# Optimization experiments

Hardware: AMD Instinct MI355X
Metric: run time of the kernel (lower is better)

Reference implementation:

```python
import jax, jax.numpy as jnp
import numpy as np

B, IN_C, W, H = 16, 1024, 32, 32
P = 256          # planes
HEADS = 4
D = P // HEADS   # 64
N = W * H
EPS = 1e-6


def setup_inputs() -> dict:
    key = jax.random.key(0)
    ks = jax.random.split(key, 12)
    s = lambda fan_in: 1.0 / np.sqrt(fan_in)
    return {
        "x": jax.random.normal(ks[0], (B, IN_C, W, H), jnp.float32),
        "w_ds": jax.random.normal(ks[1], (P, IN_C), jnp.float32) * s(IN_C),
        "wq": jax.random.normal(ks[2], (P, P), jnp.float32) * s(P),
        "bq": jax.random.normal(ks[3], (P,), jnp.float32) * 0.01,
        "wk": jax.random.normal(ks[4], (P, P), jnp.float32) * s(P),
        "bk": jax.random.normal(ks[5], (P,), jnp.float32) * 0.01,
        "wv": jax.random.normal(ks[6], (P, P), jnp.float32) * s(P),
        "bv": jax.random.normal(ks[7], (P,), jnp.float32) * 0.01,
        "rel_h": jax.random.normal(ks[8], (1, HEADS, D, 1, H), jnp.float32),
        "rel_w": jax.random.normal(ks[9], (1, HEADS, D, W, 1), jnp.float32),
        "ln_w": jnp.ones((P,), jnp.float32),
        "ln_b": jnp.zeros((P,), jnp.float32),
        "w1": jax.random.normal(ks[10], (IN_C, P), jnp.float32) * s(P),
    }


def _conv1x1(w, x, b=None):
    # w: [out, in], x: [B, in, W, H]
    y = jnp.einsum('oc,bchw->bohw', w, x)
    if b is not None:
        y = y + b[None, :, None, None]
    return y


def reference(x, w_ds, wq, bq, wk, bk, wv, bv, rel_h, rel_w, ln_w, ln_b, w1):
    out = _conv1x1(w_ds, x)  # [B, P, W, H]

    # --- MHSA ---
    q = _conv1x1(wq, out, bq).reshape(B, HEADS, D, N)
    k = _conv1x1(wk, out, bk).reshape(B, HEADS, D, N)
    v = _conv1x1(wv, out, bv).reshape(B, HEADS, D, N)

    content_content = jnp.einsum('bhdi,bhdj->bhij', q, k)  # q^T k
    pos = (rel_h + rel_w).reshape(1, HEADS, D, N)           # [1,h,d,N]
    # content_position[i,j] = pos_i . q_j  (faithful to original: matmul with q)
    content_position = jnp.einsum('xhdi,bhdj->bhij', pos, q)
    attn = jax.nn.softmax(content_content + content_position, axis=-1)
    # out[.., d, i] = sum_j v[.., d, j] * attn[.., i, j]
    o = jnp.einsum('bhdj,bhij->bhdi', v, attn).reshape(B, P, W, H)

    # --- LayerNorm (channels_last over channel dim) ---
    y = o.transpose(0, 2, 3, 1)  # [B, W, H, P]
    mu = y.mean(-1, keepdims=True)
    var = ((y - mu) ** 2).mean(-1, keepdims=True)
    y = (y - mu) / jnp.sqrt(var + EPS) * ln_w + ln_b
    y = y.transpose(0, 3, 1, 2)  # [B, P, W, H]

    # --- expand conv + exact GELU + residual ---
    out2 = jax.nn.gelu(_conv1x1(w1, y), approximate=False)
    return out2 + x
```

## Files before the change

kernel.cpp:

```cpp
#include <hip/hip_runtime.h>
#include <hip/hip_bf16.h>
#include <math.h>

#define BB 16
#define INC 1024
#define PP 256
#define NHEADS 4
#define DD 64
#define NN 1024

typedef _Float16 f16_t;
typedef __attribute__((ext_vector_type(8))) _Float16 f16x8;
typedef __attribute__((ext_vector_type(4))) _Float16 f16x4;
typedef __attribute__((ext_vector_type(4))) float f32x4;

__device__ __forceinline__ float gelu_exact(float v) {
    return 0.5f * v * (1.0f + erff(v * 0.70710678118654752440f));
}

__global__ void cast4_k(const float* __restrict__ src, f16_t* __restrict__ dst, int n4) {
    int i = blockIdx.x * 256 + threadIdx.x;
    if (i < n4) {
        float4 v = ((const float4*)src)[i];
        f16x4 o = {(f16_t)v.x, (f16_t)v.y, (f16_t)v.z, (f16_t)v.w};
        ((f16x4*)dst)[i] = o;
    }
}

__global__ __launch_bounds__(256) void transpose_xk(const float* __restrict__ x,
                                                    f16_t* __restrict__ xt) {
    __shared__ float T[64][65];
    int tid = threadIdx.x;
    int tn = tid & 63, tr = tid >> 6;
    int n0 = blockIdx.x * 64, c0 = blockIdx.y * 64;
    size_t b = blockIdx.z;
    const float* xp = x + b * 1048576;
    f16_t* xo = xt + b * 1048576;
    #pragma unroll
    for (int rr = 0; rr < 64; rr += 4)
        T[tr + rr][tn] = xp[(size_t)(c0 + tr + rr) * 1024 + n0 + tn];
    __syncthreads();
    #pragma unroll
    for (int rr = 0; rr < 64; rr += 4)
        xo[(size_t)(n0 + tr + rr) * 1024 + c0 + tn] = (f16_t)T[tn][tr + rr];
}

__global__ void pos_k(const float* __restrict__ rel_h, const float* __restrict__ rel_w,
                      f16_t* __restrict__ pos_t) {
    int idx = blockIdx.x * 256 + threadIdx.x;
    int d = idx & 63;
    int i = (idx >> 6) & 1023;
    int h = idx >> 16;
    float v = rel_h[(h * 64 + d) * 32 + (i & 31)] + rel_w[(h * 64 + d) * 32 + (i >> 5)];
    pos_t[idx] = (f16_t)v;
}

__global__ __launch_bounds__(64) void hgemm(
    const f16_t* __restrict__ A, const f16_t* __restrict__ Bt,
    const float* __restrict__ bias, const float* __restrict__ resid,
    f16_t* __restrict__ Ch, float* __restrict__ Cf,
    int M, int N, int K, int mode)
{
    int l = threadIdx.x;
    int lo = l & 15, hi = l >> 4;
    int m0 = blockIdx.y * 64;
    int n0 = blockIdx.x * 32;
    size_t b = blockIdx.z;

    const f16_t* Ap = A + (size_t)(m0 + lo) * K + hi * 8;
    const f16_t* Bq = Bt + b * (size_t)N * K + (size_t)(n0 + lo) * K + hi * 8;

    f32x4 acc[4][2] = {};

    #pragma unroll 2
    for (int k0 = 0; k0 < K; k0 += 32) {
        f16x8 bfr0 = *(const f16x8*)(Bq + k0);
        f16x8 bfr1 = *(const f16x8*)(Bq + (size_t)16 * K + k0);
        #pragma unroll
        for (int fm = 0; fm < 4; ++fm) {
            f16x8 af = *(const f16x8*)(Ap + (size_t)fm * 16 * K + k0);
            acc[fm][0] = __builtin_amdgcn_mfma_f32_16x16x32_f16(af, bfr0, acc[fm][0], 0, 0, 0);
            acc[fm][1] = __builtin_amdgcn_mfma_f32_16x16x32_f16(af, bfr1, acc[fm][1], 0, 0, 0);
        }
    }

    #pragma unroll
    for (int fn = 0; fn < 2; ++fn) {
        int n = n0 + fn * 16 + lo;
        #pragma unroll
        for (int fm = 0; fm < 4; ++fm) {
            int mb = m0 + fm * 16 + hi * 4;
            f32x4 a = acc[fm][fn];
            if (mode == 0) {
                f16x4 st;
                #pragma unroll
                for (int r = 0; r < 4; ++r) st[r] = (f16_t)a[r];
                *(f16x4*)&Ch[((size_t)b * N + n) * M + mb] = st;
            } else if (mode == 1) {
                int h = mb >> 6, d0 = mb & 63;
                f16x4 st;
                #pragma unroll
                for (int r = 0; r < 4; ++r) st[r] = (f16_t)(a[r] + bias[mb + r]);
                *(f16x4*)&Ch[(((size_t)b * 4 + h) * 1024 + n) * 64 + d0] = st;
            } else if (mode == 2) {
                int h = mb >> 6, d0 = mb & 63;
                #pragma unroll
                for (int r = 0; r < 4; ++r)
                    Ch[(((size_t)b * 4 + h) * 64 + d0 + r) * 1024 + n] = (f16_t)(a[r] + bias[mb + r]);
            } else {
                #pragma unroll
                for (int r = 0; r < 4; ++r) {
                    size_t idx = ((size_t)b * M + mb + r) * N + n;
                    Cf[idx] = gelu_exact(a[r]) + resid[idx];
                }
            }
        }
    }
}

__global__ __launch_bounds__(64) void attn_mfma(
    const f16_t* __restrict__ q_t, const f16_t* __restrict__ k_t,
    const f16_t* __restrict__ v_b, const f16_t* __restrict__ pos_t,
    float* __restrict__ o)
{
    __shared__ __align__(16) char plds[2][2048];
    int l = threadIdx.x;
    int lo = l & 15, hi = l >> 4;
    int h = blockIdx.y, b = blockIdx.z;
    int bh = b * 4 + h;
    int i_row = blockIdx.x * 32;
    size_t qbase = (size_t)bh * 1024 * 64;

    f16x8 afr[2][4];
    #pragma unroll
    for (int s = 0; s < 2; ++s) {
        const f16_t* qr = q_t + qbase + (size_t)(i_row + s * 16 + lo) * 64 + hi * 8;
        afr[s][0] = *(const f16x8*)(qr);
        afr[s][1] = *(const f16x8*)(qr + 32);
        const f16_t* pr = pos_t + ((size_t)h * 1024 + i_row + s * 16 + lo) * 64 + hi * 8;
        afr[s][2] = *(const f16x8*)(pr);
        afr[s][3] = *(const f16x8*)(pr + 32);
    }

    f32x4 acc_o[2][4] = {};
    float m_run[2][4], l_run[2][4];
    #pragma unroll
    for (int s = 0; s < 2; ++s)
        #pragma unroll
        for (int r = 0; r < 4; ++r) { m_run[s][r] = -1e30f; l_run[s][r] = 0.0f; }

    for (int j0 = 0; j0 < NN; j0 += 64) {
        f32x4 sc[2][4] = {};
        #pragma unroll
        for (int ks = 0; ks < 4; ++ks) {
            const f16_t* kb = (ks < 2 ? k_t : q_t) + qbase + (size_t)(ks & 1) * 32 + hi * 8;
            #pragma unroll
            for (int f = 0; f < 4; ++f) {
                f16x8 bf = *(const f16x8*)(kb + (size_t)(j0 + f * 16 + lo) * 64);
                sc[0][f] = __builtin_amdgcn_mfma_f32_16x16x32_f16(afr[0][ks], bf, sc[0][f], 0, 0, 0);
                sc[1][f] = __builtin_amdgcn_mfma_f32_16x16x32_f16(afr[1][ks], bf, sc[1][f], 0, 0, 0);
            }
        }
        #pragma unroll
        for (int s = 0; s < 2; ++s) {
            float mnew[4];
            #pragma unroll
            for (int r = 0; r < 4; ++r) {
                float m = fmaxf(fmaxf(sc[s][0][r], sc[s][1][r]), fmaxf(sc[s][2][r], sc[s][3][r]));
                #pragma unroll
                for (int off = 1; off < 16; off <<= 1) m = fmaxf(m, __shfl_xor(m, off, 64));
                mnew[r] = fmaxf(m_run[s][r], m);
            }
            float rsum[4] = {0.f, 0.f, 0.f, 0.f};
            #pragma unroll
            for (int f = 0; f < 4; ++f) {
                #pragma unroll
                for (int r = 0; r < 4; ++r) {
                    float p = __expf(sc[s][f][r] - mnew[r]);
                    sc[s][f][r] = p;
                    rsum[r] += p;
                }
            }
            #pragma unroll
            for (int r = 0; r < 4; ++r) {
                #pragma unroll
                for (int off = 1; off < 16; off <<= 1) rsum[r] += __shfl_xor(rsum[r], off, 64);
                float alpha = __expf(m_run[s][r] - mnew[r]);
                l_run[s][r] = l_run[s][r] * alpha + rsum[r];
                m_run[s][r] = mnew[r];
                #pragma unroll
                for (int f = 0; f < 4; ++f) acc_o[s][f][r] *= alpha;
            }
            char* pw = plds[s];
            #pragma unroll
            for (int f = 0; f < 4; ++f) {
                #pragma unroll
                for (int r = 0; r < 4; ++r) {
                    int row = hi * 4 + r;
                    int cb = (f * 16 + lo) * 2;
                    *(f16_t*)(pw + row * 128 + (cb ^ ((row & 7) << 4))) = (f16_t)sc[s][f][r];
                }
            }
        }
        asm volatile("s_waitcnt lgkmcnt(0)" ::: "memory");
        __builtin_amdgcn_sched_barrier(0);
        const f16_t* vbp = v_b + qbase + (size_t)lo * 1024 + j0 + hi * 8;
        #pragma unroll
        for (int ks = 0; ks < 2; ++ks) {
            f16x8 pa0 = *(const f16x8*)(plds[0] + lo * 128 + ((ks * 64 + hi * 16) ^ ((lo & 7) << 4)));
            f16x8 pa1 = *(const f16x8*)(plds[1] + lo * 128 + ((ks * 64 + hi * 16) ^ ((lo & 7) << 4)));
            #pragma unroll
            for (int f = 0; f < 4; ++f) {
                f16x8 vf = *(const f16x8*)(vbp + (size_t)f * 16 * 1024 + ks * 32);
                acc_o[0][f] = __builtin_amdgcn_mfma_f32_16x16x32_f16(pa0, vf, acc_o[0][f], 0, 0, 0);
                acc_o[1][f] = __builtin_amdgcn_mfma_f32_16x16x32_f16(pa1, vf, acc_o[1][f], 0, 0, 0);
            }
        }
        asm volatile("s_waitcnt lgkmcnt(0)" ::: "memory");
        __builtin_amdgcn_sched_barrier(0);
    }

    #pragma unroll
    for (int s = 0; s < 2; ++s) {
        #pragma unroll
        for (int r = 0; r < 4; ++r) {
            float inv = 1.0f / l_run[s][r];
            int n = i_row + s * 16 + hi * 4 + r;
            #pragma unroll
            for (int f = 0; f < 4; ++f) {
                o[((size_t)b * 1024 + n) * 256 + h * 64 + f * 16 + lo] = acc_o[s][f][r] * inv;
            }
        }
    }
}

__global__ __launch_bounds__(256) void ln_k(const float* __restrict__ o,
                                            f16_t* __restrict__ yt,
                                            const float* __restrict__ lw,
                                            const float* __restrict__ lb)
{
    int tid = threadIdx.x;
    int wv = tid >> 6, l = tid & 63;
    size_t row = (size_t)blockIdx.x * 4 + wv;
    f32x4 v = ((const f32x4*)(o + row * 256))[l];
    float s = v[0] + v[1] + v[2] + v[3];
    float q = v[0]*v[0] + v[1]*v[1] + v[2]*v[2] + v[3]*v[3];
    #pragma unroll
    for (int off = 1; off < 64; off <<= 1) {
        s += __shfl_xor(s, off, 64);
        q += __shfl_xor(q, off, 64);
    }
    float mean = s * (1.0f / 256.0f);
    float var = q * (1.0f / 256.0f) - mean * mean;
    float rstd = rsqrtf(var + 1e-6f);
    f32x4 w4 = ((const f32x4*)lw)[l];
    f32x4 b4 = ((const f32x4*)lb)[l];
    f16x4 o4;
    #pragma unroll
    for (int j = 0; j < 4; ++j)
        o4[j] = (f16_t)((v[j] - mean) * rstd * w4[j] + b4[j]);
    ((f16x4*)(yt + row * 256))[l] = o4;
}

extern "C" void kernel_launch(void* const* d_in, const int* in_sizes, int n_in,
                              void* d_out, int out_size, void* d_ws, size_t ws_size,
                              hipStream_t stream) {
    const float* x     = (const float*)d_in[0];
    const float* w_ds  = (const float*)d_in[1];
    const float* wq    = (const float*)d_in[2];
    const float* bq    = (const float*)d_in[3];
    const float* wk    = (const float*)d_in[4];
    const float* bk    = (const float*)d_in[5];
    const float* wv    = (const float*)d_in[6];
    const float* bv    = (const float*)d_in[7];
    const float* rel_h = (const float*)d_in[8];
    const float* rel_w = (const float*)d_in[9];
    const float* ln_w  = (const float*)d_in[10];
    const float* ln_b  = (const float*)d_in[11];
    const float* w1    = (const float*)d_in[12];
    float* out = (float*)d_out;

    f16_t* xt    = (f16_t*)d_ws;
    f16_t* wdsh  = xt + 16777216;
    f16_t* wqh   = wdsh + 262144;
    f16_t* wkh   = wqh + 65536;
    f16_t* wvh   = wkh + 65536;
    f16_t* w1h   = wvh + 65536;
    f16_t* post  = w1h + 262144;
    f16_t* out0t = post + 262144;
    f16_t* qt    = out0t + 4194304;
    f16_t* kt    = qt + 4194304;
    f16_t* vb    = kt + 4194304;
    f16_t* ytb   = vb + 4194304;
    float* ot    = (float*)(ytb + 4194304);

    cast4_k<<<256, 256, 0, stream>>>(w_ds, wdsh, 65536);
    cast4_k<<<64, 256, 0, stream>>>(wq, wqh, 16384);
    cast4_k<<<64, 256, 0, stream>>>(wk, wkh, 16384);
    cast4_k<<<64, 256, 0, stream>>>(wv, wvh, 16384);
    cast4_k<<<256, 256, 0, stream>>>(w1, w1h, 65536);
    pos_k<<<1024, 256, 0, stream>>>(rel_h, rel_w, post);
    transpose_xk<<<dim3(16, 16, 16), 256, 0, stream>>>(x, xt);

    hgemm<<<dim3(32, 4, 16), 64, 0, stream>>>(wdsh, xt, nullptr, nullptr, out0t, nullptr, PP, NN, INC, 0);
    hgemm<<<dim3(32, 4, 16), 64, 0, stream>>>(wqh, out0t, bq, nullptr, qt, nullptr, PP, NN, PP, 1);
    hgemm<<<dim3(32, 4, 16), 64, 0, stream>>>(wkh, out0t, bk, nullptr, kt, nullptr, PP, NN, PP, 1);
    hgemm<<<dim3(32, 4, 16), 64, 0, stream>>>(wvh, out0t, bv, nullptr, vb, nullptr, PP, NN, PP, 2);
    attn_mfma<<<dim3(32, 4, 16), 64, 0, stream>>>(qt, kt, vb, post, ot);
    ln_k<<<4096, 256, 0, stream>>>(ot, ytb, ln_w, ln_b);
    hgemm<<<dim3(32, 16, 16), 64, 0, stream>>>(w1h, ytb, nullptr, x, nullptr, out, INC, NN, PP, 3);
}
```

Measured before the change: 409.5 us.

## Rewrite attention with 32x32 MFMA register-resident softmax and fuse prep and QKV launches

Attention is rewritten around 32x32x16 MFMAs computing the transposed score tile. Softmax probabilities are packed to f16 in registers and exchanged by lane shuffles instead of an LDS round trip, with K/Q/V tiles double-buffered in registers and a lazy max-rescale that only fires past a threshold. The weight casts, pos table and bias packing merge into one prep kernel, and the Q/K/V projections become one 768-row GEMM launch. The x transpose now uses vectorized loads and stores, and the attention output is stored as f16, which halves LayerNorm input traffic at some precision cost.

```diff
diff --git a/kernel.cpp b/kernel.cpp
--- a/kernel.cpp
+++ b/kernel.cpp
@@ -2,73 +2,113 @@
 #include <hip/hip_bf16.h>
 #include <math.h>
 
-#define BB 16
+#define NN 1024
+#define PP 256
 #define INC 1024
-#define PP 256
-#define NHEADS 4
-#define DD 64
-#define NN 1024
 
 typedef _Float16 f16_t;
 typedef __attribute__((ext_vector_type(8))) _Float16 f16x8;
 typedef __attribute__((ext_vector_type(4))) _Float16 f16x4;
 typedef __attribute__((ext_vector_type(4))) float f32x4;
+typedef __attribute__((ext_vector_type(16))) float f32x16;
+typedef __attribute__((ext_vector_type(4))) int i32x4;
 
 __device__ __forceinline__ float gelu_exact(float v) {
     return 0.5f * v * (1.0f + erff(v * 0.70710678118654752440f));
 }
 
-__global__ void cast4_k(const float* __restrict__ src, f16_t* __restrict__ dst, int n4) {
+__device__ __forceinline__ void cvt_store(const float* __restrict__ s,
+                                          f16_t* __restrict__ d, int j) {
+    float4 v = ((const float4*)s)[j];
+    f16x4 o = {(f16_t)v.x, (f16_t)v.y, (f16_t)v.z, (f16_t)v.w};
+    ((f16x4*)d)[j] = o;
+}
+
+__global__ __launch_bounds__(256) void prep_k(
+    const float* __restrict__ w_ds, const float* __restrict__ wq,
+    const float* __restrict__ wk, const float* __restrict__ wv,
+    const float* __restrict__ w1, const float* __restrict__ rel_h,
+    const float* __restrict__ rel_w, const float* __restrict__ bq,
+    const float* __restrict__ bk, const float* __restrict__ bv,
+    f16_t* __restrict__ wdsh, f16_t* __restrict__ wqkv,
+    f16_t* __restrict__ w1h, f16_t* __restrict__ post,
+    float* __restrict__ bqkv)
+{
     int i = blockIdx.x * 256 + threadIdx.x;
-    if (i < n4) {
-        float4 v = ((const float4*)src)[i];
-        f16x4 o = {(f16_t)v.x, (f16_t)v.y, (f16_t)v.z, (f16_t)v.w};
-        ((f16x4*)dst)[i] = o;
+    if (i < 65536) {
+        cvt_store(w_ds, wdsh, i);
+    } else if (i < 81920) {
+        cvt_store(wq, wqkv, i - 65536);
+    } else if (i < 98304) {
+        cvt_store(wk, wqkv + 65536, i - 81920);
+    } else if (i < 114688) {
+        cvt_store(wv, wqkv + 131072, i - 98304);
+    } else if (i < 180224) {
+        cvt_store(w1, w1h, i - 114688);
+    } else if (i < 245760) {
+        int j = i - 180224;
+        int flat = j * 4;
+        int d = flat & 63;
+        int n = (flat >> 6) & 1023;
+        int h = flat >> 16;
+        f16x4 pk;
+        #pragma unroll
+        for (int jj = 0; jj < 4; ++jj) {
+            float v = rel_h[(h * 64 + d + jj) * 32 + (n & 31)]
+                    + rel_w[(h * 64 + d + jj) * 32 + (n >> 5)];
+            pk[jj] = (f16_t)v;
+        }
+        *(f16x4*)&post[flat] = pk;
+    } else if (i < 245952) {
+        int j = i - 245760;
+        int which = j >> 6, r = j & 63;
+        const float* src = which == 0 ? bq : (which == 1 ? bk : bv);
+        float4 v = ((const float4*)src)[r];
+        ((float4*)bqkv)[which * 64 + r] = v;
     }
 }
 
 __global__ __launch_bounds__(256) void transpose_xk(const float* __restrict__ x,
                                                     f16_t* __restrict__ xt) {
-    __shared__ float T[64][65];
+    __shared__ float T[64][68];
     int tid = threadIdx.x;
-    int tn = tid & 63, tr = tid >> 6;
     int n0 = blockIdx.x * 64, c0 = blockIdx.y * 64;
     size_t b = blockIdx.z;
     const float* xp = x + b * 1048576;
+    int cl = tid >> 4, n4 = (tid & 15) * 4;
+    #pragma unroll
+    for (int it = 0; it < 4; ++it) {
+        float4 v = *(const float4*)&xp[(size_t)(c0 + cl + it * 16) * 1024 + n0 + n4];
+        *(float4*)&T[cl + it * 16][n4] = v;
+    }
+    __syncthreads();
+    int nl = tid >> 3, ck = tid & 7;
     f16_t* xo = xt + b * 1048576;
     #pragma unroll
-    for (int rr = 0; rr < 64; rr += 4)
-        T[tr + rr][tn] = xp[(size_t)(c0 + tr + rr) * 1024 + n0 + tn];
-    __syncthreads();
-    #pragma unroll
-    for (int rr = 0; rr < 64; rr += 4)
-        xo[(size_t)(n0 + tr + rr) * 1024 + c0 + tn] = (f16_t)T[tn][tr + rr];
-}
-
-__global__ void pos_k(const float* __restrict__ rel_h, const float* __restrict__ rel_w,
-                      f16_t* __restrict__ pos_t) {
-    int idx = blockIdx.x * 256 + threadIdx.x;
-    int d = idx & 63;
-    int i = (idx >> 6) & 1023;
-    int h = idx >> 16;
-    float v = rel_h[(h * 64 + d) * 32 + (i & 31)] + rel_w[(h * 64 + d) * 32 + (i >> 5)];
-    pos_t[idx] = (f16_t)v;
+    for (int it = 0; it < 2; ++it) {
+        int n = nl + it * 32;
+        f16x8 pk;
+        #pragma unroll
+        for (int j = 0; j < 8; ++j) pk[j] = (f16_t)T[ck * 8 + j][n];
+        *(f16x8*)&xo[(size_t)(n0 + n) * 1024 + c0 + ck * 8] = pk;
+    }
 }
 
 __global__ __launch_bounds__(64) void hgemm(
     const f16_t* __restrict__ A, const f16_t* __restrict__ Bt,
     const float* __restrict__ bias, const float* __restrict__ resid,
-    f16_t* __restrict__ Ch, float* __restrict__ Cf,
+    f16_t* __restrict__ Cq, f16_t* __restrict__ Ck, f16_t* __restrict__ Cv,
+    float* __restrict__ Cf,
     int M, int N, int K, int mode)
 {
     int l = threadIdx.x;
     int lo = l & 15, hi = l >> 4;
     int m0 = blockIdx.y * 64;
     int n0 = blockIdx.x * 32;
-    size_t b = blockIdx.z;
+    size_t bb = blockIdx.z;
 
     const f16_t* Ap = A + (size_t)(m0 + lo) * K + hi * 8;
-    const f16_t* Bq = Bt + b * (size_t)N * K + (size_t)(n0 + lo) * K + hi * 8;
+    const f16_t* Bq = Bt + bb * (size_t)N * K + (size_t)(n0 + lo) * K + hi * 8;
 
     f32x4 acc[4][2] = {};
 
@@ -95,22 +135,26 @@
                 f16x4 st;
                 #pragma unroll
                 for (int r = 0; r < 4; ++r) st[r] = (f16_t)a[r];
-                *(f16x4*)&Ch[((size_t)b * N + n) * M + mb] = st;
+                *(f16x4*)&Cq[((size_t)bb * N + n) * M + mb] = st;
             } else if (mode == 1) {
-                int h = mb >> 6, d0 = mb & 63;
-                f16x4 st;
-                #pragma unroll
-                for (int r = 0; r < 4; ++r) st[r] = (f16_t)(a[r] + bias[mb + r]);
-                *(f16x4*)&Ch[(((size_t)b * 4 + h) * 1024 + n) * 64 + d0] = st;
-            } else if (mode == 2) {
-                int h = mb >> 6, d0 = mb & 63;
-                #pragma unroll
-                for (int r = 0; r < 4; ++r)
-                    Ch[(((size_t)b * 4 + h) * 64 + d0 + r) * 1024 + n] = (f16_t)(a[r] + bias[mb + r]);
+                int which = mb >> 8;
+                int mloc = mb & 255;
+                int hh = mloc >> 6, d0 = mloc & 63;
+                if (which == 2) {
+                    #pragma unroll
+                    for (int r = 0; r < 4; ++r)
+                        Cv[(((size_t)bb * 4 + hh) * 64 + d0 + r) * NN + n] = (f16_t)(a[r] + bias[mb + r]);
+                } else {
+                    f16_t* dst = which ? Ck : Cq;
+                    f16x4 st;
+                    #pragma unroll
+                    for (int r = 0; r < 4; ++r) st[r] = (f16_t)(a[r] + bias[mb + r]);
+                    *(f16x4*)&dst[(((size_t)bb * 4 + hh) * NN + n) * 64 + d0] = st;
+                }
             } else {
                 #pragma unroll
                 for (int r = 0; r < 4; ++r) {
-                    size_t idx = ((size_t)b * M + mb + r) * N + n;
+                    size_t idx = ((size_t)bb * M + mb + r) * N + n;
                     Cf[idx] = gelu_exact(a[r]) + resid[idx];
                 }
             }
@@ -121,120 +165,125 @@
 __global__ __launch_bounds__(64) void attn_mfma(
     const f16_t* __restrict__ q_t, const f16_t* __restrict__ k_t,
     const f16_t* __restrict__ v_b, const f16_t* __restrict__ pos_t,
-    float* __restrict__ o)
+    f16_t* __restrict__ o)
 {
-    __shared__ __align__(16) char plds[2][2048];
     int l = threadIdx.x;
-    int lo = l & 15, hi = l >> 4;
+    int lq = l & 31;
+    int half = l >> 5;
     int h = blockIdx.y, b = blockIdx.z;
-    int bh = b * 4 + h;
-    int i_row = blockIdx.x * 32;
-    size_t qbase = (size_t)bh * 1024 * 64;
-
-    f16x8 afr[2][4];
-    #pragma unroll
-    for (int s = 0; s < 2; ++s) {
-        const f16_t* qr = q_t + qbase + (size_t)(i_row + s * 16 + lo) * 64 + hi * 8;
-        afr[s][0] = *(const f16x8*)(qr);
-        afr[s][1] = *(const f16x8*)(qr + 32);
-        const f16_t* pr = pos_t + ((size_t)h * 1024 + i_row + s * 16 + lo) * 64 + hi * 8;
-        afr[s][2] = *(const f16x8*)(pr);
-        afr[s][3] = *(const f16x8*)(pr + 32);
-    }
-
-    f32x4 acc_o[2][4] = {};
-    float m_run[2][4], l_run[2][4];
-    #pragma unroll
-    for (int s = 0; s < 2; ++s)
-        #pragma unroll
-        for (int r = 0; r < 4; ++r) { m_run[s][r] = -1e30f; l_run[s][r] = 0.0f; }
-
-    for (int j0 = 0; j0 < NN; j0 += 64) {
-        f32x4 sc[2][4] = {};
-        #pragma unroll
-        for (int ks = 0; ks < 4; ++ks) {
-            const f16_t* kb = (ks < 2 ? k_t : q_t) + qbase + (size_t)(ks & 1) * 32 + hi * 8;
-            #pragma unroll
-            for (int f = 0; f < 4; ++f) {
-                f16x8 bf = *(const f16x8*)(kb + (size_t)(j0 + f * 16 + lo) * 64);
-                sc[0][f] = __builtin_amdgcn_mfma_f32_16x16x32_f16(afr[0][ks], bf, sc[0][f], 0, 0, 0);
-                sc[1][f] = __builtin_amdgcn_mfma_f32_16x16x32_f16(afr[1][ks], bf, sc[1][f], 0, 0, 0);
-            }
+    int q0 = blockIdx.x * 32;
+    size_t base = (size_t)(b * 4 + h) * (NN * 64);
+
+    f16x8 Bq0, Bq1, Bq2, Bq3, Bq4, Bq5, Bq6, Bq7;
+    {
+        const f16_t* qr = q_t + base + (size_t)(q0 + lq) * 64 + half * 8;
+        Bq0 = *(const f16x8*)(qr);
+        Bq1 = *(const f16x8*)(qr + 16);
+        Bq2 = *(const f16x8*)(qr + 32);
+        Bq3 = *(const f16x8*)(qr + 48);
+        const f16_t* pr = pos_t + ((size_t)h * NN + q0 + lq) * 64 + half * 8;
+        Bq4 = *(const f16x8*)(pr);
+        Bq5 = *(const f16x8*)(pr + 16);
+        Bq6 = *(const f16x8*)(pr + 32);
+        Bq7 = *(const f16x8*)(pr + 48);
+    }
+
+    f32x16 accD0 = {}, accD1 = {};
+    float m_run = -1e30f, l_run = 0.0f;
+
+    const f16_t* kbase = k_t + base + (size_t)lq * 64 + half * 8;
+    const f16_t* qbase = q_t + base + (size_t)lq * 64 + half * 8;
+    const f16_t* vbase = v_b + base + (size_t)lq * NN + half * 8;
+
+    f16x8 aK0, aK1, aK2, aK3, aQ0, aQ1, aQ2, aQ3, aV00, aV01, aV10, aV11;
+    f16x8 bK0, bK1, bK2, bK3, bQ0, bQ1, bQ2, bQ3, bV00, bV01, bV10, bV11;
+
+#define LOADT(S, J) do { \
+    const f16_t* ka_ = kbase + (size_t)(J) * 64; \
+    S##K0 = *(const f16x8*)(ka_);       S##K1 = *(const f16x8*)(ka_ + 16); \
+    S##K2 = *(const f16x8*)(ka_ + 32);  S##K3 = *(const f16x8*)(ka_ + 48); \
+    const f16_t* qa_ = qbase + (size_t)(J) * 64; \
+    S##Q0 = *(const f16x8*)(qa_);       S##Q1 = *(const f16x8*)(qa_ + 16); \
+    S##Q2 = *(const f16x8*)(qa_ + 32);  S##Q3 = *(const f16x8*)(qa_ + 48); \
+    const f16_t* va_ = vbase + (J); \
+    S##V00 = *(const f16x8*)(va_);          S##V01 = *(const f16x8*)(va_ + 16); \
+    S##V10 = *(const f16x8*)(va_ + 32 * NN); S##V11 = *(const f16x8*)(va_ + 32 * NN + 16); \
+} while (0)
+
+#define COMPUTE(S) do { \
+    f32x16 sc = {}; \
+    sc = __builtin_amdgcn_mfma_f32_32x32x16_f16(S##K0, Bq0, sc, 0, 0, 0); \
+    sc = __builtin_amdgcn_mfma_f32_32x32x16_f16(S##K1, Bq1, sc, 0, 0, 0); \
+    sc = __builtin_amdgcn_mfma_f32_32x32x16_f16(S##K2, Bq2, sc, 0, 0, 0); \
+    sc = __builtin_amdgcn_mfma_f32_32x32x16_f16(S##K3, Bq3, sc, 0, 0, 0); \
+    sc = __builtin_amdgcn_mfma_f32_32x32x16_f16(S##Q0, Bq4, sc, 0, 0, 0); \
+    sc = __builtin_amdgcn_mfma_f32_32x32x16_f16(S##Q1, Bq5, sc, 0, 0, 0); \
+    sc = __builtin_amdgcn_mfma_f32_32x32x16_f16(S##Q2, Bq6, sc, 0, 0, 0); \
+    sc = __builtin_amdgcn_mfma_f32_32x32x16_f16(S##Q3, Bq7, sc, 0, 0, 0); \
+    float mt = sc[0]; \
+    _Pragma("unroll") \
+    for (int r = 1; r < 16; ++r) mt = fmaxf(mt, sc[r]); \
+    mt = fmaxf(mt, __shfl_xor(mt, 32, 64)); \
+    if (!__all(mt <= m_run + 8.0f)) { \
+        float mnew = fmaxf(m_run, mt); \
+        float alpha = __expf(m_run - mnew); \
+        m_run = mnew; l_run *= alpha; \
+        _Pragma("unroll") \
+        for (int r = 0; r < 16; ++r) { accD0[r] *= alpha; accD1[r] *= alpha; } \
+    } \
+    float p[16]; float rs = 0.0f; \
+    _Pragma("unroll") \
+    for (int r = 0; r < 16; ++r) { p[r] = __expf(sc[r] - m_run); rs += p[r]; } \
+    rs += __shfl_xor(rs, 32, 64); \
+    l_run += rs; \
+    int w0 = __builtin_bit_cast(int, __builtin_amdgcn_cvt_pkrtz(p[0], p[1])); \
+    int w1 = __builtin_bit_cast(int, __builtin_amdgcn_cvt_pkrtz(p[2], p[3])); \
+    int w2 = __builtin_bit_cast(int, __builtin_amdgcn_cvt_pkrtz(p[4], p[5])); \
+    int w3 = __builtin_bit_cast(int, __builtin_amdgcn_cvt_pkrtz(p[6], p[7])); \
+    int w4 = __builtin_bit_cast(int, __builtin_amdgcn_cvt_pkrtz(p[8], p[9])); \
+    int w5 = __builtin_bit_cast(int, __builtin_amdgcn_cvt_pkrtz(p[10], p[11])); \
+    int w6 = __builtin_bit_cast(int, __builtin_amdgcn_cvt_pkrtz(p[12], p[13])); \
+    int w7 = __builtin_bit_cast(int, __builtin_amdgcn_cvt_pkrtz(p[14], p[15])); \
+    int x0 = __shfl_xor(w0, 32, 64), x1 = __shfl_xor(w1, 32, 64); \
+    int x2 = __shfl_xor(w2, 32, 64), x3 = __shfl_xor(w3, 32, 64); \
+    int x4 = __shfl_xor(w4, 32, 64), x5 = __shfl_xor(w5, 32, 64); \
+    int x6 = __shfl_xor(w6, 32, 64), x7 = __shfl_xor(w7, 32, 64); \
+    i32x4 pb0 = { half ? x2 : w0, half ? x3 : w1, half ? w2 : x0, half ? w3 : x1 }; \
+    i32x4 pb1 = { half ? x6 : w4, half ? x7 : w5, half ? w6 : x4, half ? w7 : x5 }; \
+    f16x8 Pf0 = __builtin_bit_cast(f16x8, pb0); \
+    f16x8 Pf1 = __builtin_bit_cast(f16x8, pb1); \
+    accD0 = __builtin_amdgcn_mfma_f32_32x32x16_f16(S##V00, Pf0, accD0, 0, 0, 0); \
+    accD0 = __builtin_amdgcn_mfma_f32_32x32x16_f16(S##V01, Pf1, accD0, 0, 0, 0); \
+    accD1 = __builtin_amdgcn_mfma_f32_32x32x16_f16(S##V10, Pf0, accD1, 0, 0, 0); \
+    accD1 = __builtin_amdgcn_mfma_f32_32x32x16_f16(S##V11, Pf1, accD1, 0, 0, 0); \
+} while (0)
+
+    LOADT(a, 0);
+    for (int t = 0; t < 32; t += 2) {
+        LOADT(b, (t + 1) * 32);
+        COMPUTE(a);
+        LOADT(a, (size_t)(((t + 2) & 31) * 32));
+        COMPUTE(b);
+    }
+#undef LOADT
+#undef COMPUTE
+
+    float inv = 1.0f / l_run;
+    size_t orow = ((size_t)b * NN + q0 + lq) * 256 + h * 64;
+    #pragma unroll
+    for (int rg = 0; rg < 4; ++rg) {
+        f16x4 s0, s1;
+        #pragma unroll
+        for (int c = 0; c < 4; ++c) {
+            s0[c] = (f16_t)(accD0[rg * 4 + c] * inv);
+            s1[c] = (f16_t)(accD1[rg * 4 + c] * inv);
         }
-        #pragma unroll
-        for (int s = 0; s < 2; ++s) {
-            float mnew[4];
-            #pragma unroll
-            for (int r = 0; r < 4; ++r) {
-                float m = fmaxf(fmaxf(sc[s][0][r], sc[s][1][r]), fmaxf(sc[s][2][r], sc[s][3][r]));
-                #pragma unroll
-                for (int off = 1; off < 16; off <<= 1) m = fmaxf(m, __shfl_xor(m, off, 64));
-                mnew[r] = fmaxf(m_run[s][r], m);
-            }
-            float rsum[4] = {0.f, 0.f, 0.f, 0.f};
-            #pragma unroll
-            for (int f = 0; f < 4; ++f) {
-                #pragma unroll
-                for (int r = 0; r < 4; ++r) {
-                    float p = __expf(sc[s][f][r] - mnew[r]);
-                    sc[s][f][r] = p;
-                    rsum[r] += p;
-                }
-            }
-            #pragma unroll
-            for (int r = 0; r < 4; ++r) {
-                #pragma unroll
-                for (int off = 1; off < 16; off <<= 1) rsum[r] += __shfl_xor(rsum[r], off, 64);
-                float alpha = __expf(m_run[s][r] - mnew[r]);
-                l_run[s][r] = l_run[s][r] * alpha + rsum[r];
-                m_run[s][r] = mnew[r];
-                #pragma unroll
-                for (int f = 0; f < 4; ++f) acc_o[s][f][r] *= alpha;
-            }
-            char* pw = plds[s];
-            #pragma unroll
-            for (int f = 0; f < 4; ++f) {
-                #pragma unroll
-                for (int r = 0; r < 4; ++r) {
-                    int row = hi * 4 + r;
-                    int cb = (f * 16 + lo) * 2;
-                    *(f16_t*)(pw + row * 128 + (cb ^ ((row & 7) << 4))) = (f16_t)sc[s][f][r];
-                }
-            }
-        }
-        asm volatile("s_waitcnt lgkmcnt(0)" ::: "memory");
-        __builtin_amdgcn_sched_barrier(0);
-        const f16_t* vbp = v_b + qbase + (size_t)lo * 1024 + j0 + hi * 8;
-        #pragma unroll
-        for (int ks = 0; ks < 2; ++ks) {
-            f16x8 pa0 = *(const f16x8*)(plds[0] + lo * 128 + ((ks * 64 + hi * 16) ^ ((lo & 7) << 4)));
-            f16x8 pa1 = *(const f16x8*)(plds[1] + lo * 128 + ((ks * 64 + hi * 16) ^ ((lo & 7) << 4)));
-            #pragma unroll
-            for (int f = 0; f < 4; ++f) {
-                f16x8 vf = *(const f16x8*)(vbp + (size_t)f * 16 * 1024 + ks * 32);
-                acc_o[0][f] = __builtin_amdgcn_mfma_f32_16x16x32_f16(pa0, vf, acc_o[0][f], 0, 0, 0);
-                acc_o[1][f] = __builtin_amdgcn_mfma_f32_16x16x32_f16(pa1, vf, acc_o[1][f], 0, 0, 0);
-            }
-        }
-        asm volatile("s_waitcnt lgkmcnt(0)" ::: "memory");
-        __builtin_amdgcn_sched_barrier(0);
-    }
-
-    #pragma unroll
-    for (int s = 0; s < 2; ++s) {
-        #pragma unroll
-        for (int r = 0; r < 4; ++r) {
-            float inv = 1.0f / l_run[s][r];
-            int n = i_row + s * 16 + hi * 4 + r;
-            #pragma unroll
-            for (int f = 0; f < 4; ++f) {
-                o[((size_t)b * 1024 + n) * 256 + h * 64 + f * 16 + lo] = acc_o[s][f][r] * inv;
-            }
-        }
-    }
-}
-
-__global__ __launch_bounds__(256) void ln_k(const float* __restrict__ o,
+        *(f16x4*)&o[orow + rg * 8 + half * 4] = s0;
+        *(f16x4*)&o[orow + 32 + rg * 8 + half * 4] = s1;
+    }
+}
+
+__global__ __launch_bounds__(256) void ln_k(const f16_t* __restrict__ o,
                                             f16_t* __restrict__ yt,
                                             const float* __restrict__ lw,
                                             const float* __restrict__ lb)
@@ -242,7 +291,10 @@
     int tid = threadIdx.x;
     int wv = tid >> 6, l = tid & 63;
     size_t row = (size_t)blockIdx.x * 4 + wv;
-    f32x4 v = ((const f32x4*)(o + row * 256))[l];
+    f16x4 v4 = ((const f16x4*)(o + row * 256))[l];
+    float v[4];
+    #pragma unroll
+    for (int j = 0; j < 4; ++j) v[j] = (float)v4[j];
     float s = v[0] + v[1] + v[2] + v[3];
     float q = v[0]*v[0] + v[1]*v[1] + v[2]*v[2] + v[3]*v[3];
     #pragma unroll
@@ -282,31 +334,30 @@
 
     f16_t* xt    = (f16_t*)d_ws;
     f16_t* wdsh  = xt + 16777216;
-    f16_t* wqh   = wdsh + 262144;
-    f16_t* wkh   = wqh + 65536;
-    f16_t* wvh   = wkh + 65536;
-    f16_t* w1h   = wvh + 65536;
+    f16_t* wqkv  = wdsh + 262144;
+    f16_t* w1h   = wqkv + 196608;
     f16_t* post  = w1h + 262144;
     f16_t* out0t = post + 262144;
     f16_t* qt    = out0t + 4194304;
     f16_t* kt    = qt + 4194304;
     f16_t* vb    = kt + 4194304;
     f16_t* ytb   = vb + 4194304;
-    float* ot    = (float*)(ytb + 4194304);
-
-    cast4_k<<<256, 256, 0, stream>>>(w_ds, wdsh, 65536);
-    cast4_k<<<64, 256, 0, stream>>>(wq, wqh, 16384);
-    cast4_k<<<64, 256, 0, stream>>>(wk, wkh, 16384);
-    cast4_k<<<64, 256, 0, stream>>>(wv, wvh, 16384);
-    cast4_k<<<256, 256, 0, stream>>>(w1, w1h, 65536);
-    pos_k<<<1024, 256, 0, stream>>>(rel_h, rel_w, post);
+    f16_t* oat   = ytb + 4194304;
+    float* bqkv  = (float*)(oat + 4194304);
+
+    prep_k<<<961, 256, 0, stream>>>(w_ds, wq, wk, wv, w1, rel_h, rel_w,
+                                    bq, bk, bv, wdsh, wqkv, w1h, post, bqkv);
     transpose_xk<<<dim3(16, 16, 16), 256, 0, stream>>>(x, xt);
 
-    hgemm<<<dim3(32, 4, 16), 64, 0, stream>>>(wdsh, xt, nullptr, nullptr, out0t, nullptr, PP, NN, INC, 0);
-    hgemm<<<dim3(32, 4, 16), 64, 0, stream>>>(wqh, out0t, bq, nullptr, qt, nullptr, PP, NN, PP, 1);
-    hgemm<<<dim3(32, 4, 16), 64, 0, stream>>>(wkh, out0t, bk, nullptr, kt, nullptr, PP, NN, PP, 1);
-    hgemm<<<dim3(32, 4, 16), 64, 0, stream>>>(wvh, out0t, bv, nullptr, vb, nullptr, PP, NN, PP, 2);
-    attn_mfma<<<dim3(32, 4, 16), 64, 0, stream>>>(qt, kt, vb, post, ot);
-    ln_k<<<4096, 256, 0, stream>>>(ot, ytb, ln_w, ln_b);
-    hgemm<<<dim3(32, 16, 16), 64, 0, stream>>>(w1h, ytb, nullptr, x, nullptr, out, INC, NN, PP, 3);
-}
+    hgemm<<<dim3(32, 4, 16), 64, 0, stream>>>(wdsh, xt, nullptr, nullptr,
+                                              out0t, nullptr, nullptr, nullptr,
+                                              PP, NN, INC, 0);
+    hgemm<<<dim3(32, 12, 16), 64, 0, stream>>>(wqkv, out0t, bqkv, nullptr,
+                                               qt, kt, vb, nullptr,
+                                               768, NN, PP, 1);
+    attn_mfma<<<dim3(32, 4, 16), 64, 0, stream>>>(qt, kt, vb, post, oat);
+    ln_k<<<4096, 256, 0, stream>>>(oat, ytb, ln_w, ln_b);
+    hgemm<<<dim3(32, 16, 16), 64, 0, stream>>>(w1h, ytb, nullptr, x,
+                                               nullptr, nullptr, nullptr, out,
+                                               INC, NN, PP, 3);
+}
```

New measurement: 396.6 us. 1.03x faster.
